# Performance work log

Hardware: AMD Instinct MI355X
Metric: run time of the kernel (lower is better)

The kernel has to match this reference:

```python
import jax, jax.numpy as jnp
import numpy as np

E = 1024   # embedding_size
K = 64     # key_size
DH = 64    # head_size
H = 16     # layer_size (num heads)
F = 4096   # hidden_size
B, S = 4, 2048
EPS = float(np.finfo(np.float32).eps)  # torch RMSNorm default eps


def setup_inputs() -> dict:
    key = jax.random.key(0)
    ks = jax.random.split(key, 12)
    embeddings = jax.random.normal(ks[0], (B, S, E), dtype=jnp.float32)
    # causal additive mask: 0 on/below diagonal, -1e9 above
    tri = jnp.triu(jnp.ones((S, S), dtype=bool), k=1)
    causal_buffer = jnp.where(tri, -1e9, 0.0).astype(jnp.float32)[None]  # [1,S,S]
    # standard RoPE cos/sin buffers over the key dim
    inv_freq = 1.0 / (10000.0 ** (jnp.arange(0, K // 2, dtype=jnp.float32) * 2.0 / K))
    ang = jnp.arange(S, dtype=jnp.float32)[:, None] * inv_freq[None, :]  # [S,K/2]
    ang = jnp.concatenate([ang, ang], axis=-1)                           # [S,K]
    cos_buffer = jnp.cos(ang)[None]  # [1,S,K]
    sin_buffer = jnp.sin(ang)[None]
    sc = 0.02
    wq = jax.random.normal(ks[1], (H, E, K), dtype=jnp.float32) * sc
    wk = jax.random.normal(ks[2], (H, E, K), dtype=jnp.float32) * sc
    wv = jax.random.normal(ks[3], (H, E, DH), dtype=jnp.float32) * sc
    w_proj = jax.random.normal(ks[4], (E, E), dtype=jnp.float32) * sc
    attn_norm_w = jnp.ones((E,), dtype=jnp.float32)
    mlp_norm_w = jnp.ones((E,), dtype=jnp.float32)
    w_up = jax.random.normal(ks[5], (E, F), dtype=jnp.float32) * sc
    w_gate = jax.random.normal(ks[6], (E, F), dtype=jnp.float32) * sc
    w_down = jax.random.normal(ks[7], (F, E), dtype=jnp.float32) * sc
    return {"embeddings": embeddings, "causal_buffer": causal_buffer,
            "cos_buffer": cos_buffer, "sin_buffer": sin_buffer,
            "wq": wq, "wk": wk, "wv": wv, "w_proj": w_proj,
            "attn_norm_w": attn_norm_w, "mlp_norm_w": mlp_norm_w,
            "w_up": w_up, "w_gate": w_gate, "w_down": w_down}


def _rmsnorm(x, w):
    ms = jnp.mean(x * x, axis=-1, keepdims=True)
    return x * jax.lax.rsqrt(ms + EPS) * w


def _rotate(x, cos, sin):
    # x: [B,H,S,K]; cos/sin: [1,1,S,K]. swapped = cat(second_half, first_half)
    swapped = jnp.concatenate([x[..., K // 2:], x[..., :K // 2]], axis=-1)
    return cos * x + sin * swapped


def reference(embeddings, causal_buffer, cos_buffer, sin_buffer,
              wq, wk, wv, w_proj, attn_norm_w, mlp_norm_w,
              w_up, w_gate, w_down):
    cos = cos_buffer[:, None]  # [1,1,S,K]
    sin = sin_buffer[:, None]
    # NOTE: original computes attention_norm(embeddings) but feeds RAW
    # embeddings to the heads; we reproduce that faithfully.
    q = _rotate(jnp.einsum('bse,hek->bhsk', embeddings, wq), cos, sin)
    k = _rotate(jnp.einsum('bse,hek->bhsk', embeddings, wk), cos, sin)
    v = jnp.einsum('bse,hed->bhsd', embeddings, wv)
    scores = jnp.einsum('bhsk,bhtk->bhst', q, k) / jnp.sqrt(jnp.float32(K))
    scores = scores + causal_buffer[:, None]  # broadcast over heads
    weights = jax.nn.softmax(scores, axis=-1)
    attn = jnp.einsum('bhst,bhtd->bhsd', weights, v)  # [B,H,S,DH]
    attn = attn.transpose(0, 2, 1, 3).reshape(attn.shape[0], attn.shape[2], H * DH)
    x = embeddings + attn @ w_proj
    h = _rmsnorm(x, mlp_norm_w)
    mlp = (h @ w_up) * jax.nn.elu(h @ w_gate)
    return x + mlp @ w_down
```

## Files before the change

kernel.cpp:

```cpp
#include <hip/hip_runtime.h>
#include <cstdint>
#include <cstddef>

#define E_DIM 1024
#define S_LEN 2048
#define NB 4
#define NH 16
#define F_DIM 4096

typedef __attribute__((ext_vector_type(8))) __bf16 bf16x8;
typedef __attribute__((ext_vector_type(4))) __bf16 bf16x4;
typedef __attribute__((ext_vector_type(4))) float f32x4;
typedef __attribute__((ext_vector_type(16))) float f32x16;

__device__ __forceinline__ f32x4 mfma16(bf16x8 a, bf16x8 b, f32x4 c) {
  return __builtin_amdgcn_mfma_f32_16x16x32_bf16(a, b, c, 0, 0, 0);
}
__device__ __forceinline__ f32x16 mfma32(bf16x8 a, bf16x8 b, f32x16 c) {
  return __builtin_amdgcn_mfma_f32_32x32x16_bf16(a, b, c, 0, 0, 0);
}

__device__ __forceinline__ unsigned short f2bf(float f) {
  __bf16 h = (__bf16)f;
  return __builtin_bit_cast(unsigned short, h);
}

__device__ __forceinline__ void gl_lds16(const void* gptr, void* lptr) {
  __builtin_amdgcn_global_load_lds(
      (const __attribute__((address_space(1))) void*)gptr,
      (__attribute__((address_space(3))) void*)lptr, 16, 0, 0);
}


__global__ __launch_bounds__(256) void cast_emb_kernel(
    const float4* __restrict__ in, ushort4* __restrict__ out) {
  int i = blockIdx.x * 256 + threadIdx.x;
  float4 v = in[i];
  ushort4 o;
  o.x = f2bf(v.x); o.y = f2bf(v.y); o.z = f2bf(v.z); o.w = f2bf(v.w);
  out[i] = o;
}

__global__ __launch_bounds__(256) void transpose_cast_kernel(
    const float* __restrict__ in, unsigned short* __restrict__ out, int R, int C) {
  __shared__ float tile[32][33];
  const int bz = blockIdx.z;
  const float* ip = in + (size_t)bz * R * C;
  const int r0 = blockIdx.y * 32, c0 = blockIdx.x * 32;
  const int tc = threadIdx.x & 31, tr = threadIdx.x >> 5;
#pragma unroll
  for (int i = 0; i < 4; ++i)
    tile[tr + i * 8][tc] = ip[(size_t)(r0 + tr + i * 8) * C + (c0 + tc)];
  __syncthreads();
#pragma unroll
  for (int i = 0; i < 4; ++i)
    out[(size_t)(bz * C + c0 + tr + i * 8) * R + (r0 + tc)] = f2bf(tile[tc][tr + i * 8]);
}

__global__ __launch_bounds__(256) void transpose_cast_qkv(
    const float* __restrict__ wq, const float* __restrict__ wk,
    const float* __restrict__ wv, unsigned short* __restrict__ out) {
  __shared__ float tile[32][33];
  const int bz = blockIdx.z;
  const int which = bz >> 4, hz = bz & 15;
  const float* ip =
      (which == 0 ? wq : which == 1 ? wk : wv) + (size_t)hz * 1024 * 64;
  unsigned short* op = out + (size_t)which * 1024 * 1024;
  const int r0 = blockIdx.y * 32, c0 = blockIdx.x * 32;
  const int tc = threadIdx.x & 31, tr = threadIdx.x >> 5;
#pragma unroll
  for (int i = 0; i < 4; ++i)
    tile[tr + i * 8][tc] = ip[(size_t)(r0 + tr + i * 8) * 64 + (c0 + tc)];
  __syncthreads();
#pragma unroll
  for (int i = 0; i < 4; ++i)
    op[(size_t)(hz * 64 + c0 + tr + i * 8) * 1024 + (r0 + tc)] =
        f2bf(tile[tc][tr + i * 8]);
}

__global__ __launch_bounds__(256) void transpose_cast_upgate(
    const float* __restrict__ wup, const float* __restrict__ wgate,
    unsigned short* __restrict__ out) {
  __shared__ float tile[32][33];
  const int z = blockIdx.z & 1;
  const float* ip = z ? wgate : wup;
  const int r0 = blockIdx.y * 32, c0 = blockIdx.x * 32;
  const int tc = threadIdx.x & 31, tr = threadIdx.x >> 5;
#pragma unroll
  for (int i = 0; i < 4; ++i)
    tile[tr + i * 8][tc] = ip[(size_t)(r0 + tr + i * 8) * F_DIM + (c0 + tc)];
  __syncthreads();
#pragma unroll
  for (int i = 0; i < 4; ++i) {
    const int c = c0 + tr + i * 8;
    const int row = 64 * (c >> 5) + (c & 31) + z * 32;
    out[(size_t)row * E_DIM + (r0 + tc)] = f2bf(tile[tc][tr + i * 8]);
  }
}

template <int EPI, int KD>
__global__ __launch_bounds__(256) void gemm_bt(
    const unsigned short* __restrict__ A, const unsigned short* __restrict__ Bt,
    const float* __restrict__ aux, float* __restrict__ fout) {
  __shared__ unsigned short As[128 * 64];
  __shared__ unsigned short Bs[128 * 64];
  const int t = threadIdx.x;
  const int lane = t & 63, w = t >> 6;
  const int l31 = lane & 31, half = lane >> 5;
  const int wm = (w >> 1) * 64, wn = (w & 1) * 64;
  const int m0 = blockIdx.y * 128, n0 = blockIdx.x * 128;
  const int sr = t >> 3, sc = t & 7;
  const int gcoff = (sc ^ (sr & 7)) * 8;
  const unsigned short* ga = A + (size_t)(m0 + sr) * KD + gcoff;
  const unsigned short* gb = Bt + (size_t)(n0 + sr) * KD + gcoff;
  unsigned short* lA = &As[sr * 64 + sc * 8];
  unsigned short* lB = &Bs[sr * 64 + sc * 8];
  const int xh = lane & 7;
  f32x16 acc[2][2] = {};
  for (int k0 = 0; k0 < KD; k0 += 64) {
    __syncthreads();
#pragma unroll
    for (int i = 0; i < 4; ++i) {
      gl_lds16(ga + (size_t)(i * 32) * KD + k0, lA + i * 32 * 64);
      gl_lds16(gb + (size_t)(i * 32) * KD + k0, lB + i * 32 * 64);
    }
    __syncthreads();
#pragma unroll
    for (int ksl = 0; ksl < 4; ++ksl) {
      const int cp = ((ksl * 2 + half) ^ xh) * 8;
      bf16x8 af[2], bfr[2];
#pragma unroll
      for (int mi = 0; mi < 2; ++mi)
        af[mi] = *reinterpret_cast<const bf16x8*>(&As[(wm + mi * 32 + l31) * 64 + cp]);
#pragma unroll
      for (int ni = 0; ni < 2; ++ni)
        bfr[ni] = *reinterpret_cast<const bf16x8*>(&Bs[(wn + ni * 32 + l31) * 64 + cp]);
#pragma unroll
      for (int mi = 0; mi < 2; ++mi)
#pragma unroll
        for (int ni = 0; ni < 2; ++ni)
          acc[mi][ni] = mfma32(af[mi], bfr[ni], acc[mi][ni]);
    }
  }
#pragma unroll
  for (int mi = 0; mi < 2; ++mi)
#pragma unroll
    for (int ni = 0; ni < 2; ++ni) {
      const int n = n0 + wn + ni * 32 + l31;
#pragma unroll
      for (int reg = 0; reg < 16; ++reg) {
        const int m = m0 + wm + mi * 32 + (reg & 3) + 8 * (reg >> 2) + 4 * half;
        const size_t idx = (size_t)m * 1024 + n;
        fout[idx] = aux[idx] + acc[mi][ni][reg];
      }
    }
}

#define FENCE() asm volatile("" ::: "memory")
#define BARX()                        \
  do {                                \
    FENCE();                          \
    __builtin_amdgcn_s_barrier();     \
    FENCE();                          \
  } while (0)
#define VMW_(n) asm volatile("s_waitcnt vmcnt(" #n ")" ::: "memory")
#define VMW(n) VMW_(n)

template <int EPI>
__global__ __launch_bounds__(512, 2) void gemm256(
    const unsigned short* __restrict__ A, const unsigned short* __restrict__ Bt,
    const float* __restrict__ cosb, const float* __restrict__ sinb,
    unsigned short* __restrict__ qout, unsigned short* __restrict__ kout,
    unsigned short* __restrict__ vtout, unsigned short* __restrict__ gout) {
  constexpr int KD = 1024;
  constexpr int NT = KD / 64;
  __shared__ unsigned short L[8 * 8192];
  const int tid = threadIdx.x;
  const int lane = tid & 63, w = tid >> 6;
  const int l31 = lane & 31, half = lane >> 5;
  const int wm = (w >> 2) * 128, wn = (w & 3) * 64;
  int m0, n0;
  if (EPI == 0) {
    const int f = blockIdx.y * 12 + blockIdx.x;
    const int fl = (f & 7) * 48 + (f >> 3);
    m0 = (fl / 12) * 256;
    n0 = (fl % 12) * 256;
  } else {
    m0 = blockIdx.y * 256;
    n0 = blockIdx.x * 256;
  }
  const int r = tid >> 2;
  const int csrc = ((tid & 3) ^ ((r ^ (r >> 2)) & 3)) * 8;
  const unsigned short* gA = A + (size_t)(m0 + r) * KD + csrc;
  const unsigned short* gB = Bt + (size_t)(n0 + r) * KD + csrc;
  const int ldst = tid * 8;
  const int sA = (l31 ^ (l31 >> 2)) & 3;

  f32x16 acc[4][2] = {};
  bf16x8 a[4], b[2];

#define STG(ridx, gp, koff)                                                    \
  do {                                                                         \
    gl_lds16((gp) + (koff), &L[(ridx) * 8192 + ldst]);                         \
    gl_lds16((gp) + (koff) + (size_t)128 * KD,                                 \
             &L[(ridx) * 8192 + 4096 + ldst]);                                 \
  } while (0)

#define RD(hh, kl, bufi)                                                       \
  do {                                                                         \
    const int xo = ((((kl) * 2 + half) ^ sA)) * 8;                             \
    const int ra = ((bufi) * 4 + 1 + 2 * (hh)) * 8192;                         \
    const int rb = ((bufi) * 4 + 2 * (hh)) * 8192;                             \
    _Pragma("unroll") for (int mi = 0; mi < 4; ++mi)                           \
        a[mi] = *reinterpret_cast<const bf16x8*>(                              \
            &L[ra + (wm + mi * 32 + l31) * 32 + xo]);                          \
    _Pragma("unroll") for (int ni = 0; ni < 2; ++ni)                           \
        b[ni] = *reinterpret_cast<const bf16x8*>(                              \
            &L[rb + (wn + ni * 32 + l31) * 32 + xo]);                          \
  } while (0)

#define MFMA8()                                                                \
  do {                                                                         \
    __builtin_amdgcn_s_setprio(1);                                             \
    _Pragma("unroll") for (int mi = 0; mi < 4; ++mi)                           \
        _Pragma("unroll") for (int ni = 0; ni < 2; ++ni)                       \
            acc[mi][ni] = mfma32(a[mi], b[ni], acc[mi][ni]);                   \
    __builtin_amdgcn_s_setprio(0);                                             \
  } while (0)

  STG(0, gB, 0); FENCE();
  STG(1, gA, 0); FENCE();
  STG(2, gB, 32); FENCE();
  STG(3, gA, 32); FENCE();

  int buf = 0;
  for (int t = 0; t < NT; ++t, buf ^= 1) {
    const int nx = buf ^ 1;
    const bool pre = (t + 1 < NT);
    const int ko = (t + 1) * 64;
    VMW(4);
    BARX();
    RD(0, 0, buf);
    if (pre) STG(nx * 4 + 0, gB, ko);
    MFMA8();
    BARX();
    RD(0, 1, buf);
    if (pre) STG(nx * 4 + 1, gA, ko);
    MFMA8();
    if (pre) {
      VMW(4);
    } else {
      VMW(0);
    }
    BARX();
    RD(1, 0, buf);
    if (pre) STG(nx * 4 + 2, gB, ko + 32);
    MFMA8();
    BARX();
    RD(1, 1, buf);
    if (pre) STG(nx * 4 + 3, gA, ko + 32);
    MFMA8();
  }

  if (EPI == 3) {
    const int colb = ((n0 + wn) >> 1) + l31;
#pragma unroll
    for (int mi = 0; mi < 4; ++mi)
#pragma unroll
      for (int reg = 0; reg < 16; ++reg) {
        const int m = m0 + wm + mi * 32 + (reg & 3) + 8 * (reg >> 2) + 4 * half;
        const float uu = acc[mi][0][reg], gg = acc[mi][1][reg];
        const float e = gg > 0.f ? gg : (__expf(gg) - 1.f);
        gout[(size_t)m * F_DIM + colb] = f2bf(uu * e);
      }
  } else {
    const int seg = n0 >> 10;
    const int nl = (n0 & 1023) + wn;
    if (seg == 2) {
#pragma unroll
      for (int mi = 0; mi < 4; ++mi)
#pragma unroll
        for (int ni = 0; ni < 2; ++ni) {
          const int rest = nl + ni * 32 + l31;
          const int hh = rest >> 6, kk = rest & 63;
#pragma unroll
          for (int g = 0; g < 4; ++g) {
            const int m = m0 + wm + mi * 32 + 8 * g + 4 * half;
            const int bb = m >> 11, s = m & 2047;
            ushort4 pk;
            pk.x = f2bf(acc[mi][ni][g * 4 + 0]);
            pk.y = f2bf(acc[mi][ni][g * 4 + 1]);
            pk.z = f2bf(acc[mi][ni][g * 4 + 2]);
            pk.w = f2bf(acc[mi][ni][g * 4 + 3]);
            *reinterpret_cast<ushort4*>(
                &vtout[(((size_t)(bb * NH + hh)) * 64 + kk) * S_LEN + s]) = pk;
          }
        }
    } else {
      unsigned short* dst = (seg == 0) ? qout : kout;
      const float scl = (seg == 0) ? 0.125f : 1.0f;
#pragma unroll
      for (int mi = 0; mi < 4; ++mi)
#pragma unroll
        for (int ni = 0; ni < 2; ++ni) {
          const int rest = nl + ni * 32 + l31;
          const int hh = rest >> 6, kk = rest & 63;
#pragma unroll
          for (int reg = 0; reg < 16; ++reg) {
            const int m =
                m0 + wm + mi * 32 + (reg & 3) + 8 * (reg >> 2) + 4 * half;
            const int bb = m >> 11, s = m & 2047;
            const float v = acc[mi][ni][reg];
            const float sw = acc[mi][ni ^ 1][reg];
            const float cv = cosb[s * 64 + kk], sv = sinb[s * 64 + kk];
            dst[(((size_t)(bb * NH + hh)) * S_LEN + s) * 64 + kk] =
                f2bf((cv * v + sv * sw) * scl);
          }
        }
    }
  }
#undef STG
#undef RD
#undef MFMA8
}

__global__ __launch_bounds__(256, 1) void gemm_down(
    const unsigned short* __restrict__ A, const unsigned short* __restrict__ Bt,
    const float* __restrict__ aux, float* __restrict__ fout) {
  constexpr int KD = 4096;
  constexpr int NT = KD / 64;
  __shared__ unsigned short L[3 * 24576];
  const int tid = threadIdx.x;
  const int lane = tid & 63, w = tid >> 6;
  const int l31 = lane & 31, half = lane >> 5;
  const int wm = (w >> 1) * 128, wn = (w & 1) * 64;
  const int f = blockIdx.y * 8 + blockIdx.x;
  const int xcd = f & 7, loc = f >> 3;
  const int m0 = (xcd * 4 + (loc >> 3)) * 256;
  const int n0 = (loc & 7) * 128;
  const int r = tid >> 2;
  const int csrc = ((tid & 3) ^ ((r ^ (r >> 2)) & 3)) * 8;
  const unsigned short* gA = A + (size_t)(m0 + r) * KD + csrc;
  const unsigned short* gB = Bt + (size_t)(n0 + r) * KD + csrc;
  const int ldst = tid * 8;
  const int sA = (l31 ^ (l31 >> 2)) & 3;

  f32x16 acc[4][2] = {};
  bf16x8 a[4], b[2];

#define STG_HALF(hh, tt, bufw)                                                 \
  do {                                                                         \
    const size_t ko = (size_t)(tt) * 64 + (hh) * 32;                           \
    unsigned short* Lb = &L[(bufw) * 24576 + (hh) * 12288];                    \
    gl_lds16(gB + ko, Lb + ldst);                                              \
    gl_lds16(gB + ko + (size_t)64 * KD, Lb + 2048 + ldst);                     \
    gl_lds16(gA + ko, Lb + 4096 + ldst);                                       \
    gl_lds16(gA + ko + (size_t)64 * KD, Lb + 6144 + ldst);                     \
    gl_lds16(gA + ko + (size_t)128 * KD, Lb + 8192 + ldst);                    \
    gl_lds16(gA + ko + (size_t)192 * KD, Lb + 10240 + ldst);                   \
    FENCE();                                                                   \
  } while (0)

#define RDF(kl, hh, base_)                                                     \
  do {                                                                         \
    const int xo = (((kl) * 2 + half) ^ sA) * 8;                               \
    const unsigned short* Lr = &L[(base_) + (hh) * 12288];                     \
    _Pragma("unroll") for (int ni = 0; ni < 2; ++ni)                           \
        b[ni] = *reinterpret_cast<const bf16x8*>(                              \
            &Lr[(wn + ni * 32 + l31) * 32 + xo]);                              \
    _Pragma("unroll") for (int mi = 0; mi < 4; ++mi)                           \
        a[mi] = *reinterpret_cast<const bf16x8*>(                              \
            &Lr[4096 + (wm + mi * 32 + l31) * 32 + xo]);                       \
  } while (0)

#define MFMA8D()                                                               \
  do {                                                                         \
    __builtin_amdgcn_s_setprio(1);                                             \
    _Pragma("unroll") for (int mi = 0; mi < 4; ++mi)                           \
        _Pragma("unroll") for (int ni = 0; ni < 2; ++ni)                       \
            acc[mi][ni] = mfma32(a[mi], b[ni], acc[mi][ni]);                   \
    __builtin_amdgcn_s_setprio(0);                                             \
  } while (0)

#define PHASED(hh, bufr, VM, tt_issue, bufw, DO_ISSUE)                         \
  do {                                                                         \
    VMW(VM);                                                                   \
    BARX();                                                                    \
    const int base_ = (bufr) * 24576;                                          \
    RDF(0, hh, base_);                                                         \
    if (DO_ISSUE) STG_HALF(hh, tt_issue, bufw);                                \
    MFMA8D();                                                                  \
    RDF(1, hh, base_);                                                         \
    MFMA8D();                                                                  \
  } while (0)

  STG_HALF(0, 0, 0);
  STG_HALF(1, 0, 0);
  STG_HALF(0, 1, 1);
  STG_HALF(1, 1, 1);

  int br = 0;
  for (int t = 0; t < NT - 2; ++t) {
    const int bw = (br >= 1) ? br - 1 : br + 2;
    PHASED(0, br, 18, t + 2, bw, true);
    PHASED(1, br, 18, t + 2, bw, true);
    br = (br == 2) ? 0 : br + 1;
  }
  PHASED(0, br, 18, 0, 0, false);
  PHASED(1, br, 12, 0, 0, false);
  br = (br == 2) ? 0 : br + 1;
  PHASED(0, br, 6, 0, 0, false);
  PHASED(1, br, 0, 0, 0, false);

#pragma unroll
  for (int mi = 0; mi < 4; ++mi)
#pragma unroll
    for (int ni = 0; ni < 2; ++ni) {
      const int n = n0 + wn + ni * 32 + l31;
#pragma unroll
      for (int reg = 0; reg < 16; ++reg) {
        const int m = m0 + wm + mi * 32 + (reg & 3) + 8 * (reg >> 2) + 4 * half;
        const size_t idx = (size_t)m * 1024 + n;
        fout[idx] = aux[idx] + acc[mi][ni][reg];
      }
    }
#undef STG_HALF
#undef RDF
#undef MFMA8D
#undef PHASED
}

#define PS_STRIDE 68
__global__ __launch_bounds__(256) void flash_attn(
    const unsigned short* __restrict__ qb, const unsigned short* __restrict__ kb,
    const unsigned short* __restrict__ vtb, unsigned short* __restrict__ attn) {
  __shared__ unsigned short Ks[64 * 64];
  __shared__ unsigned short Vts[64 * 64];
  __shared__ unsigned short Ps[128 * PS_STRIDE];
  const int t = threadIdx.x, lane = t & 63, w = t >> 6;
  const int quad = lane >> 4, l15 = lane & 15;
  const int qt = 15 - blockIdx.y;
  const int bh = blockIdx.x;
  const int b = bh >> 4, hh = bh & 15;
  const unsigned short* qg = qb + (size_t)bh * S_LEN * 64;
  const unsigned short* kg = kb + (size_t)bh * S_LEN * 64;
  const unsigned short* vg = vtb + (size_t)bh * 64 * S_LEN;
  bf16x8 aq[2][2];
#pragma unroll
  for (int mi = 0; mi < 2; ++mi)
#pragma unroll
    for (int ks = 0; ks < 2; ++ks)
      aq[mi][ks] = *reinterpret_cast<const bf16x8*>(
          qg + (size_t)(qt * 128 + w * 32 + mi * 16 + l15) * 64 + ks * 32 + quad * 8);
  f32x4 o[2][4] = {};
  float lpart[2][4] = {};
  const int srk = t >> 3, sck = t & 7;
  const int gck = ((sck ^ (srk & 7)) * 8);
  const int xh = l15 & 7;
  const int ktmax = 2 * qt + 1;
  for (int kt = 0; kt <= ktmax; ++kt) {
    __syncthreads();
#pragma unroll
    for (int i = 0; i < 2; ++i) {
      gl_lds16(kg + (size_t)(kt * 64 + srk + i * 32) * 64 + gck,
               &Ks[(srk + i * 32) * 64 + sck * 8]);
      gl_lds16(vg + (size_t)(srk + i * 32) * S_LEN + kt * 64 + gck,
               &Vts[(srk + i * 32) * 64 + sck * 8]);
    }
    __syncthreads();
    f32x4 sacc[2][4];
#pragma unroll
    for (int mi = 0; mi < 2; ++mi)
#pragma unroll
      for (int nt = 0; nt < 4; ++nt) sacc[mi][nt] = (f32x4){-8.f, -8.f, -8.f, -8.f};
#pragma unroll
    for (int nt = 0; nt < 4; ++nt) {
      bf16x8 b0 = *reinterpret_cast<const bf16x8*>(
          &Ks[(nt * 16 + l15) * 64 + ((quad ^ xh) * 8)]);
      bf16x8 b1 = *reinterpret_cast<const bf16x8*>(
          &Ks[(nt * 16 + l15) * 64 + (((4 + quad) ^ xh) * 8)]);
#pragma unroll
      for (int mi = 0; mi < 2; ++mi) {
        sacc[mi][nt] = mfma16(aq[mi][0], b0, sacc[mi][nt]);
        sacc[mi][nt] = mfma16(aq[mi][1], b1, sacc[mi][nt]);
      }
    }
    if (kt >= 2 * qt) {
#pragma unroll
      for (int mi = 0; mi < 2; ++mi)
#pragma unroll
        for (int nt = 0; nt < 4; ++nt)
#pragma unroll
          for (int rg = 0; rg < 4; ++rg) {
            const int row = qt * 128 + w * 32 + mi * 16 + quad * 4 + rg;
            const int col = kt * 64 + nt * 16 + l15;
            if (col > row) sacc[mi][nt][rg] = -1e9f;
          }
    }
#pragma unroll
    for (int mi = 0; mi < 2; ++mi)
#pragma unroll
      for (int nt = 0; nt < 4; ++nt)
#pragma unroll
        for (int rg = 0; rg < 4; ++rg) {
          const float p = __expf(sacc[mi][nt][rg]);
          lpart[mi][rg] += p;
          Ps[(w * 32 + mi * 16 + quad * 4 + rg) * PS_STRIDE + nt * 16 + l15] = f2bf(p);
        }
#pragma unroll
    for (int ks = 0; ks < 2; ++ks) {
      bf16x8 ap[2];
#pragma unroll
      for (int mi = 0; mi < 2; ++mi) {
        const unsigned short* pp =
            &Ps[(w * 32 + mi * 16 + l15) * PS_STRIDE + ks * 32 + quad * 8];
        bf16x4 lo = *reinterpret_cast<const bf16x4*>(pp);
        bf16x4 hi = *reinterpret_cast<const bf16x4*>(pp + 4);
        ap[mi] = __builtin_shufflevector(lo, hi, 0, 1, 2, 3, 4, 5, 6, 7);
      }
#pragma unroll
      for (int vt = 0; vt < 4; ++vt) {
        bf16x8 bv = *reinterpret_cast<const bf16x8*>(
            &Vts[(vt * 16 + l15) * 64 + (((ks * 4 + quad) ^ xh) * 8)]);
#pragma unroll
        for (int mi = 0; mi < 2; ++mi) o[mi][vt] = mfma16(ap[mi], bv, o[mi][vt]);
      }
    }
  }
  float linv[2][4];
#pragma unroll
  for (int mi = 0; mi < 2; ++mi)
#pragma unroll
    for (int rg = 0; rg < 4; ++rg) {
      float rs = lpart[mi][rg];
#pragma unroll
      for (int d = 1; d < 16; d <<= 1) rs += __shfl_xor(rs, d);
      linv[mi][rg] = 1.0f / rs;
    }
#pragma unroll
  for (int mi = 0; mi < 2; ++mi)
#pragma unroll
    for (int vt = 0; vt < 4; ++vt)
#pragma unroll
      for (int rg = 0; rg < 4; ++rg) {
        const int row = w * 32 + mi * 16 + quad * 4 + rg;
        const int s = qt * 128 + row;
        const float ov = o[mi][vt][rg] * linv[mi][rg];
        attn[((size_t)(b * S_LEN + s)) * E_DIM + hh * 64 + vt * 16 + l15] = f2bf(ov);
      }
}

__global__ __launch_bounds__(256) void rmsnorm_kernel(
    const float* __restrict__ x, const float* __restrict__ wgt,
    unsigned short* __restrict__ hout) {
  const int row = blockIdx.x;
  const int t = threadIdx.x;
  const float4 v = reinterpret_cast<const float4*>(x + (size_t)row * E_DIM)[t];
  float ss = v.x * v.x + v.y * v.y + v.z * v.z + v.w * v.w;
#pragma unroll
  for (int d = 1; d < 64; d <<= 1) ss += __shfl_xor(ss, d);
  __shared__ float red[4];
  if ((t & 63) == 0) red[t >> 6] = ss;
  __syncthreads();
  const float tot = red[0] + red[1] + red[2] + red[3];
  const float sc = rsqrtf(tot * (1.f / 1024.f) + 1.1920929e-07f);
  const float4 g = reinterpret_cast<const float4*>(wgt)[t];
  ushort4 ov;
  ov.x = f2bf(v.x * sc * g.x);
  ov.y = f2bf(v.y * sc * g.y);
  ov.z = f2bf(v.z * sc * g.z);
  ov.w = f2bf(v.w * sc * g.w);
  reinterpret_cast<ushort4*>(hout + (size_t)row * E_DIM)[t] = ov;
}

extern "C" void kernel_launch(void* const* d_in, const int* in_sizes, int n_in,
                              void* d_out, int out_size, void* d_ws, size_t ws_size,
                              hipStream_t stream) {
  (void)in_sizes; (void)n_in; (void)out_size; (void)ws_size;
  const float* emb = (const float*)d_in[0];
  const float* cosb = (const float*)d_in[2];
  const float* sinb = (const float*)d_in[3];
  const float* wq = (const float*)d_in[4];
  const float* wk = (const float*)d_in[5];
  const float* wv = (const float*)d_in[6];
  const float* wproj = (const float*)d_in[7];
  const float* mlpw = (const float*)d_in[9];
  const float* wup = (const float*)d_in[10];
  const float* wgate = (const float*)d_in[11];
  const float* wdown = (const float*)d_in[12];
  float* out = (float*)d_out;
  char* ws = (char*)d_ws;
  unsigned short* wqkv_t = (unsigned short*)(ws + 0);
  unsigned short* wproj_t = (unsigned short*)(ws + 6291456);
  unsigned short* wupgate_t = (unsigned short*)(ws + 8388608);
  unsigned short* wdown_t = (unsigned short*)(ws + 25165824);
  unsigned short* embb = (unsigned short*)(ws + 33554432);
  unsigned short* qbuf = (unsigned short*)(ws + 50331648);
  unsigned short* kbuf = (unsigned short*)(ws + 67108864);
  unsigned short* vtbuf = (unsigned short*)(ws + 83886080);
  unsigned short* gbuf = (unsigned short*)(ws + 33554432);
  unsigned short* attnb = (unsigned short*)(ws + 100663296);
  float* xbuf = (float*)(ws + 117440512);
  unsigned short* hbuf = (unsigned short*)(ws + 150994944);

  dim3 blk(256);
  cast_emb_kernel<<<8192, blk, 0, stream>>>((const float4*)emb, (ushort4*)embb);
  transpose_cast_qkv<<<dim3(2, 32, 48), blk, 0, stream>>>(wq, wk, wv, wqkv_t);
  transpose_cast_kernel<<<dim3(32, 32, 1), blk, 0, stream>>>(wproj, wproj_t, 1024, 1024);
  transpose_cast_upgate<<<dim3(128, 32, 2), blk, 0, stream>>>(wup, wgate, wupgate_t);
  transpose_cast_kernel<<<dim3(32, 128, 1), blk, 0, stream>>>(wdown, wdown_t, 4096, 1024);
  gemm256<0><<<dim3(12, 32), dim3(512), 0, stream>>>(
      embb, wqkv_t, cosb, sinb, qbuf, kbuf, vtbuf, nullptr);
  flash_attn<<<dim3(64, 16), blk, 0, stream>>>(qbuf, kbuf, vtbuf, attnb);
  gemm_bt<1, 1024><<<dim3(8, 64), blk, 0, stream>>>(attnb, wproj_t, emb, xbuf);
  rmsnorm_kernel<<<8192, blk, 0, stream>>>(xbuf, mlpw, hbuf);
  gemm256<3><<<dim3(32, 32), dim3(512), 0, stream>>>(
      hbuf, wupgate_t, nullptr, nullptr, nullptr, nullptr, nullptr, gbuf);
  gemm_down<<<dim3(8, 32), blk, 0, stream>>>(gbuf, wdown_t, xbuf, out);
}
```

Measured before the change: 555.7 us.

## Use 4-wave 256x256 GEMM blocks with 128x128 per-wave tiles

The 256x256 tile GEMM now runs with 256 threads (4 waves) instead of 512 (8 waves). Each wave computes a 128x128 sub-tile with a 4x4 accumulator array, which gives more MFMA reuse per LDS fragment read. Each half-K step now loads two k-slices at once, so the loop has half as many barriers. The cost is many more accumulator registers per wave and a 1-block-per-CU launch bound, which lowers occupancy and reduces latency hiding. Each thread also issues more global-to-LDS loads.

```diff
diff --git a/kernel.cpp b/kernel.cpp
--- a/kernel.cpp
+++ b/kernel.cpp
@@ -167,7 +167,7 @@
 #define VMW(n) VMW_(n)
 
 template <int EPI>
-__global__ __launch_bounds__(512, 2) void gemm256(
+__global__ __launch_bounds__(256, 1) void gemm256(
     const unsigned short* __restrict__ A, const unsigned short* __restrict__ Bt,
     const float* __restrict__ cosb, const float* __restrict__ sinb,
     unsigned short* __restrict__ qout, unsigned short* __restrict__ kout,
@@ -178,7 +178,7 @@
   const int tid = threadIdx.x;
   const int lane = tid & 63, w = tid >> 6;
   const int l31 = lane & 31, half = lane >> 5;
-  const int wm = (w >> 2) * 128, wn = (w & 3) * 64;
+  const int wm = (w >> 1) * 128, wn = (w & 1) * 128;
   int m0, n0;
   if (EPI == 0) {
     const int f = blockIdx.y * 12 + blockIdx.x;
@@ -196,70 +196,78 @@
   const int ldst = tid * 8;
   const int sA = (l31 ^ (l31 >> 2)) & 3;
 
-  f32x16 acc[4][2] = {};
-  bf16x8 a[4], b[2];
+  f32x16 acc[4][4] = {};
+  bf16x8 a0[4], a1[4], b0[4], b1[4];
 
 #define STG(ridx, gp, koff)                                                    \
   do {                                                                         \
     gl_lds16((gp) + (koff), &L[(ridx) * 8192 + ldst]);                         \
+    gl_lds16((gp) + (koff) + (size_t)64 * KD,                                  \
+             &L[(ridx) * 8192 + 2048 + ldst]);                                 \
     gl_lds16((gp) + (koff) + (size_t)128 * KD,                                 \
              &L[(ridx) * 8192 + 4096 + ldst]);                                 \
-  } while (0)
-
-#define RD(hh, kl, bufi)                                                       \
+    gl_lds16((gp) + (koff) + (size_t)192 * KD,                                 \
+             &L[(ridx) * 8192 + 6144 + ldst]);                                 \
+    FENCE();                                                                   \
+  } while (0)
+
+#define RDH(hh, bufi)                                                          \
   do {                                                                         \
-    const int xo = ((((kl) * 2 + half) ^ sA)) * 8;                             \
-    const int ra = ((bufi) * 4 + 1 + 2 * (hh)) * 8192;                         \
-    const int rb = ((bufi) * 4 + 2 * (hh)) * 8192;                             \
-    _Pragma("unroll") for (int mi = 0; mi < 4; ++mi)                           \
-        a[mi] = *reinterpret_cast<const bf16x8*>(                              \
-            &L[ra + (wm + mi * 32 + l31) * 32 + xo]);                          \
-    _Pragma("unroll") for (int ni = 0; ni < 2; ++ni)                           \
-        b[ni] = *reinterpret_cast<const bf16x8*>(                              \
-            &L[rb + (wn + ni * 32 + l31) * 32 + xo]);                          \
-  } while (0)
-
-#define MFMA8()                                                                \
+    const int ra_ = ((bufi) * 4 + 1 + 2 * (hh)) * 8192;                        \
+    const int rb_ = ((bufi) * 4 + 2 * (hh)) * 8192;                            \
+    const int xo0_ = (half ^ sA) * 8;                                          \
+    const int xo1_ = ((2 + half) ^ sA) * 8;                                    \
+    _Pragma("unroll") for (int mi = 0; mi < 4; ++mi) {                         \
+      a0[mi] = *reinterpret_cast<const bf16x8*>(                               \
+          &L[ra_ + (wm + mi * 32 + l31) * 32 + xo0_]);                         \
+      a1[mi] = *reinterpret_cast<const bf16x8*>(                               \
+          &L[ra_ + (wm + mi * 32 + l31) * 32 + xo1_]);                         \
+    }                                                                          \
+    _Pragma("unroll") for (int ni = 0; ni < 4; ++ni) {                         \
+      b0[ni] = *reinterpret_cast<const bf16x8*>(                               \
+          &L[rb_ + (wn + ni * 32 + l31) * 32 + xo0_]);                         \
+      b1[ni] = *reinterpret_cast<const bf16x8*>(                               \
+          &L[rb_ + (wn + ni * 32 + l31) * 32 + xo1_]);                         \
+    }                                                                          \
+  } while (0)
+
+#define MFMAC(aa, bb)                                                          \
   do {                                                                         \
     __builtin_amdgcn_s_setprio(1);                                             \
     _Pragma("unroll") for (int mi = 0; mi < 4; ++mi)                           \
-        _Pragma("unroll") for (int ni = 0; ni < 2; ++ni)                       \
-            acc[mi][ni] = mfma32(a[mi], b[ni], acc[mi][ni]);                   \
+        _Pragma("unroll") for (int ni = 0; ni < 4; ++ni)                       \
+            acc[mi][ni] = mfma32(aa[mi], bb[ni], acc[mi][ni]);                 \
     __builtin_amdgcn_s_setprio(0);                                             \
   } while (0)
 
-  STG(0, gB, 0); FENCE();
-  STG(1, gA, 0); FENCE();
-  STG(2, gB, 32); FENCE();
-  STG(3, gA, 32); FENCE();
+  STG(0, gB, 0);
+  STG(1, gA, 0);
+  STG(2, gB, 32);
+  STG(3, gA, 32);
 
   int buf = 0;
   for (int t = 0; t < NT; ++t, buf ^= 1) {
     const int nx = buf ^ 1;
     const bool pre = (t + 1 < NT);
     const int ko = (t + 1) * 64;
-    VMW(4);
+    VMW(8);
     BARX();
-    RD(0, 0, buf);
-    if (pre) STG(nx * 4 + 0, gB, ko);
-    MFMA8();
+    RDH(0, buf);
+    if (pre) {
+      STG(nx * 4 + 0, gB, ko);
+      STG(nx * 4 + 1, gA, ko);
+    }
+    MFMAC(a0, b0);
+    MFMAC(a1, b1);
+    if (pre) { VMW(8); } else { VMW(0); }
     BARX();
-    RD(0, 1, buf);
-    if (pre) STG(nx * 4 + 1, gA, ko);
-    MFMA8();
+    RDH(1, buf);
     if (pre) {
-      VMW(4);
-    } else {
-      VMW(0);
-    }
-    BARX();
-    RD(1, 0, buf);
-    if (pre) STG(nx * 4 + 2, gB, ko + 32);
-    MFMA8();
-    BARX();
-    RD(1, 1, buf);
-    if (pre) STG(nx * 4 + 3, gA, ko + 32);
-    MFMA8();
+      STG(nx * 4 + 2, gB, ko + 32);
+      STG(nx * 4 + 3, gA, ko + 32);
+    }
+    MFMAC(a0, b0);
+    MFMAC(a1, b1);
   }
 
   if (EPI == 3) {
@@ -267,12 +275,14 @@
 #pragma unroll
     for (int mi = 0; mi < 4; ++mi)
 #pragma unroll
-      for (int reg = 0; reg < 16; ++reg) {
-        const int m = m0 + wm + mi * 32 + (reg & 3) + 8 * (reg >> 2) + 4 * half;
-        const float uu = acc[mi][0][reg], gg = acc[mi][1][reg];
-        const float e = gg > 0.f ? gg : (__expf(gg) - 1.f);
-        gout[(size_t)m * F_DIM + colb] = f2bf(uu * e);
-      }
+      for (int p = 0; p < 2; ++p)
+#pragma unroll
+        for (int reg = 0; reg < 16; ++reg) {
+          const int m = m0 + wm + mi * 32 + (reg & 3) + 8 * (reg >> 2) + 4 * half;
+          const float uu = acc[mi][2 * p][reg], gg = acc[mi][2 * p + 1][reg];
+          const float e = gg > 0.f ? gg : (__expf(gg) - 1.f);
+          gout[(size_t)m * F_DIM + colb + p * 32] = f2bf(uu * e);
+        }
   } else {
     const int seg = n0 >> 10;
     const int nl = (n0 & 1023) + wn;
@@ -280,7 +290,7 @@
 #pragma unroll
       for (int mi = 0; mi < 4; ++mi)
 #pragma unroll
-        for (int ni = 0; ni < 2; ++ni) {
+        for (int ni = 0; ni < 4; ++ni) {
           const int rest = nl + ni * 32 + l31;
           const int hh = rest >> 6, kk = rest & 63;
 #pragma unroll
@@ -302,7 +312,7 @@
 #pragma unroll
       for (int mi = 0; mi < 4; ++mi)
 #pragma unroll
-        for (int ni = 0; ni < 2; ++ni) {
+        for (int ni = 0; ni < 4; ++ni) {
           const int rest = nl + ni * 32 + l31;
           const int hh = rest >> 6, kk = rest & 63;
 #pragma unroll
@@ -320,8 +330,8 @@
     }
   }
 #undef STG
-#undef RD
-#undef MFMA8
+#undef RDH
+#undef MFMAC
 }
 
 __global__ __launch_bounds__(256, 1) void gemm_down(
@@ -609,12 +619,12 @@
   transpose_cast_kernel<<<dim3(32, 32, 1), blk, 0, stream>>>(wproj, wproj_t, 1024, 1024);
   transpose_cast_upgate<<<dim3(128, 32, 2), blk, 0, stream>>>(wup, wgate, wupgate_t);
   transpose_cast_kernel<<<dim3(32, 128, 1), blk, 0, stream>>>(wdown, wdown_t, 4096, 1024);
-  gemm256<0><<<dim3(12, 32), dim3(512), 0, stream>>>(
+  gemm256<0><<<dim3(12, 32), dim3(256), 0, stream>>>(
       embb, wqkv_t, cosb, sinb, qbuf, kbuf, vtbuf, nullptr);
   flash_attn<<<dim3(64, 16), blk, 0, stream>>>(qbuf, kbuf, vtbuf, attnb);
   gemm_bt<1, 1024><<<dim3(8, 64), blk, 0, stream>>>(attnb, wproj_t, emb, xbuf);
   rmsnorm_kernel<<<8192, blk, 0, stream>>>(xbuf, mlpw, hbuf);
-  gemm256<3><<<dim3(32, 32), dim3(512), 0, stream>>>(
+  gemm256<3><<<dim3(32, 32), dim3(256), 0, stream>>>(
       hbuf, wupgate_t, nullptr, nullptr, nullptr, nullptr, nullptr, gbuf);
   gemm_down<<<dim3(8, 32), blk, 0, stream>>>(gbuf, wdown_t, xbuf, out);
 }
```

New measurement: 677.0 us. +21.8%, slower.
